# Kernel optimization log

Hardware: AMD Instinct MI355X
Metric: run time of the kernel (lower is better)

The kernel has to match this reference:

```python
import jax, jax.numpy as jnp
import numpy as np

B, J, PD = 4, 6890, 3
D, L, H, DH = 256, 4, 8, 64
INNER = H * DH          # 512
N = 2048                # downsample_dim (token count)
FF = 1024
M = 13780               # num_joints * upsample
HEAD_OUT = [3, 1, 3, 4, 3]  # mean3D, opacity, shs, rotations, scales


def setup_inputs() -> dict:
    ks = jax.random.split(jax.random.key(0), 16)
    rn = lambda k, shape, s=0.05: jax.random.normal(k, shape, jnp.float32) * s
    z = lambda shape: jnp.zeros(shape, jnp.float32)
    o = lambda shape: jnp.ones(shape, jnp.float32)
    return {
        'x': rn(ks[0], (B, J, PD), 1.0),
        'pre_emb_w': rn(ks[1], (PD, D)), 'pre_emb_b': z((D,)),
        'pre_conv_w': rn(ks[2], (N, J)), 'pre_conv_b': z((N,)),
        'pos_emb': rn(ks[3], (N, D), 0.02),
        'pre_norm_g': o((D,)), 'pre_norm_b': z((D,)),
        'ln1_g': o((L, D)), 'ln1_b': z((L, D)),
        'qkv_w': rn(ks[4], (L, D, 3 * INNER)),
        'out_w': rn(ks[5], (L, INNER, D)), 'out_b': z((L, D)),
        'ln2_g': o((L, D)), 'ln2_b': z((L, D)),
        'ff_w1': rn(ks[6], (L, D, FF)), 'ff_b1': z((L, FF)),
        'ff_w2': rn(ks[7], (L, FF, D)), 'ff_b2': z((L, D)),
        'up_w': rn(ks[8], (M, N)), 'up_b': z((M,)),
        'heads_w1': rn(ks[9], (5, D, D)), 'heads_b1': z((5, D)),
        'heads_w2': rn(ks[10], (5, D, 4)), 'heads_b2': z((5, 4)),
    }


def _ln(x, g, b, eps=1e-5):
    mu = jnp.mean(x, -1, keepdims=True)
    var = jnp.mean(jnp.square(x - mu), -1, keepdims=True)
    return (x - mu) * jax.lax.rsqrt(var + eps) * g + b


def _gelu(x):
    return jax.nn.gelu(x, approximate=False)  # torch nn.GELU default (erf)


def reference(x, pre_emb_w, pre_emb_b, pre_conv_w, pre_conv_b, pos_emb,
              pre_norm_g, pre_norm_b, ln1_g, ln1_b, qkv_w, out_w, out_b,
              ln2_g, ln2_b, ff_w1, ff_b1, ff_w2, ff_b2, up_w, up_b,
              heads_w1, heads_b1, heads_w2, heads_b2):
    scale = DH ** -0.5
    # token embedding: Linear(pose_dim->hidden) then Conv1d(num_joints->downsample_dim, k=1)
    h = x @ pre_emb_w + pre_emb_b                               # [B,J,D]
    h = jnp.einsum('bjd,nj->bnd', h, pre_conv_w) + pre_conv_b[None, :, None]  # [B,N,D]
    h = h + pos_emb[None]                                       # positional embedding
    h = _ln(h, pre_norm_g, pre_norm_b)
    # transformer encoder (pre-norm self-attn + FFN, residual)
    for i in range(L):
        y = _ln(h, ln1_g[i], ln1_b[i])
        qkv = y @ qkv_w[i]                                      # [B,N,3*INNER]
        q, k, v = jnp.split(qkv, 3, axis=-1)
        q = q.reshape(B, N, H, DH).transpose(0, 2, 1, 3)        # [B,H,N,DH]
        k = k.reshape(B, N, H, DH).transpose(0, 2, 1, 3)
        v = v.reshape(B, N, H, DH).transpose(0, 2, 1, 3)
        dots = jnp.einsum('bhnd,bhmd->bhnm', q, k) * scale      # [B,H,N,N]
        attn = jax.nn.softmax(dots, axis=-1)
        o = jnp.einsum('bhnm,bhmd->bhnd', attn, v)
        o = o.transpose(0, 2, 1, 3).reshape(B, N, INNER)
        h = o @ out_w[i] + out_b[i] + h
        y = _ln(h, ln2_g[i], ln2_b[i])
        h = _gelu(y @ ff_w1[i] + ff_b1[i]) @ ff_w2[i] + ff_b2[i] + h
    # upsample conv: Conv1d(downsample_dim -> num_joints*upsample, k=1)
    u = jnp.einsum('bnd,mn->bmd', h, up_w) + up_b[None, :, None]  # [B,M,D]
    # 5 gaussian-attribute heads (stacked; out dims padded to 4 and sliced)
    hid = _gelu(jnp.einsum('bmd,kde->kbme', u, heads_w1) + heads_b1[:, None, None, :])
    op = jnp.einsum('kbme,keo->kbmo', hid, heads_w2) + heads_b2[:, None, None, :]
    outs = [op[i, ..., :HEAD_OUT[i]] for i in range(5)]
    return jnp.concatenate(outs, axis=-1)                       # [B,M,14]
```

## Files before the change

kernel.cpp:

```cpp
#include <hip/hip_runtime.h>
#include <math.h>

#define B_ 4
#define J_ 6890
#define D_ 256
#define L_ 4
#define H_ 8
#define DH_ 64
#define INNER_ 512
#define N_ 2048
#define FF_ 1024
#define M_ 13780
#define MP_ 13824

typedef float4 f4;
typedef __attribute__((ext_vector_type(8))) short s16x8;
typedef __attribute__((ext_vector_type(4))) float fx4;

__device__ __forceinline__ float b2f(short s) {
    return __uint_as_float(((unsigned int)(unsigned short)s) << 16);
}
__device__ __forceinline__ short f2bf(float f) {
    unsigned int u = __float_as_uint(f);
    unsigned int r = (u + 0x7FFFu + ((u >> 16) & 1u)) >> 16;
    return (short)r;
}
__device__ __forceinline__ float gelu_f(float v) {
    return 0.5f * v * (1.0f + erff(v * 0.70710678118654752440f));
}

__device__ __forceinline__ void gld16(void* lds, const void* g) {
    __builtin_amdgcn_global_load_lds(
        (const __attribute__((address_space(1))) void*)g,
        (__attribute__((address_space(3))) void*)lds, 16, 0, 0);
}

__global__ __launch_bounds__(256) void embed_ln_kernel(
    const float* __restrict__ x, const float* __restrict__ emb_w,
    const float* __restrict__ emb_b, const float* __restrict__ conv_w,
    const float* __restrict__ conv_b, const float* __restrict__ pos_emb,
    const float* __restrict__ g, const float* __restrict__ beta,
    float* __restrict__ hout)
{
    const int n = blockIdx.x, b = blockIdx.y, t = threadIdx.x;
    const float* wrow = conv_w + (size_t)n * J_;
    const float* xb = x + (size_t)b * J_ * 3;
    float t0 = 0.f, t1 = 0.f, t2 = 0.f, s = 0.f;
    for (int j = t; j < J_; j += 256) {
        float w = wrow[j];
        s  += w;
        t0 += w * xb[3*j+0];
        t1 += w * xb[3*j+1];
        t2 += w * xb[3*j+2];
    }
    __shared__ float red[16];
    #pragma unroll
    for (int off = 32; off > 0; off >>= 1) {
        t0 += __shfl_down(t0, off, 64);
        t1 += __shfl_down(t1, off, 64);
        t2 += __shfl_down(t2, off, 64);
        s  += __shfl_down(s,  off, 64);
    }
    const int lane = t & 63, wid = t >> 6;
    if (lane == 0) { red[wid*4+0]=t0; red[wid*4+1]=t1; red[wid*4+2]=t2; red[wid*4+3]=s; }
    __syncthreads();
    t0 = red[0]+red[4]+red[8]+red[12];
    t1 = red[1]+red[5]+red[9]+red[13];
    t2 = red[2]+red[6]+red[10]+red[14];
    s  = red[3]+red[7]+red[11]+red[15];
    __syncthreads();

    float val = t0*emb_w[t] + t1*emb_w[D_+t] + t2*emb_w[2*D_+t]
              + s*emb_b[t] + conv_b[n] + pos_emb[(size_t)n*D_ + t];

    float sv = val, sq = val*val;
    #pragma unroll
    for (int off = 32; off > 0; off >>= 1) {
        sv += __shfl_down(sv, off, 64);
        sq += __shfl_down(sq, off, 64);
    }
    if (lane == 0) { red[wid*2]=sv; red[wid*2+1]=sq; }
    __syncthreads();
    sv = red[0]+red[2]+red[4]+red[6];
    sq = red[1]+red[3]+red[5]+red[7];
    float mu   = sv * (1.f/D_);
    float var  = sq * (1.f/D_) - mu*mu;
    float rstd = rsqrtf(fmaxf(var, 0.f) + 1e-5f);
    hout[((size_t)(b*N_ + n))*D_ + t] = (val - mu)*rstd*g[t] + beta[t];
}

__global__ __launch_bounds__(256) void ln_bf_kernel(
    const float* __restrict__ in, short* __restrict__ outp,
    const float* __restrict__ g, const float* __restrict__ beta)
{
    const int row = blockIdx.x, t = threadIdx.x;
    float v = in[(size_t)row*D_ + t];
    float sv = v, sq = v*v;
    #pragma unroll
    for (int off = 32; off > 0; off >>= 1) {
        sv += __shfl_down(sv, off, 64);
        sq += __shfl_down(sq, off, 64);
    }
    __shared__ float red[8];
    const int lane = t & 63, wid = t >> 6;
    if (lane == 0) { red[wid*2]=sv; red[wid*2+1]=sq; }
    __syncthreads();
    sv = red[0]+red[2]+red[4]+red[6];
    sq = red[1]+red[3]+red[5]+red[7];
    float mu   = sv * (1.f/D_);
    float var  = sq * (1.f/D_) - mu*mu;
    float rstd = rsqrtf(fmaxf(var, 0.f) + 1e-5f);
    outp[(size_t)row*D_ + t] = f2bf((v - mu)*rstd*g[t] + beta[t]);
}

__global__ __launch_bounds__(256) void tcvt_kernel(
    const float* __restrict__ in, short* __restrict__ outp,
    int R, int C, long inZ, long outZ)
{
    in   += (size_t)blockIdx.z * inZ;
    outp += (size_t)blockIdx.z * outZ;
    __shared__ float tile[32][33];
    const int c0 = blockIdx.x * 32, r0 = blockIdx.y * 32;
    const int t = threadIdx.x;
    const int row = t >> 3, c4 = (t & 7) * 4;
    f4 v = *(const f4*)&in[(size_t)(r0 + row)*C + c0 + c4];
    tile[row][c4+0] = v.x; tile[row][c4+1] = v.y;
    tile[row][c4+2] = v.z; tile[row][c4+3] = v.w;
    __syncthreads();
    const int oc = t >> 3, r4 = (t & 7) * 4;
    short* dst = &outp[(size_t)(c0 + oc)*R + r0 + r4];
    #pragma unroll
    for (int j = 0; j < 4; j++) dst[j] = f2bf(tile[r4 + j][oc]);
}

__global__ __launch_bounds__(256) void cvt_kernel(
    const float* __restrict__ in, short* __restrict__ outp)
{
    const size_t i = ((size_t)blockIdx.x * 256 + threadIdx.x) * 8;
    f4 a = *(const f4*)&in[i];
    f4 b = *(const f4*)&in[i + 4];
    s16x8 s;
    s[0]=f2bf(a.x); s[1]=f2bf(a.y); s[2]=f2bf(a.z); s[3]=f2bf(a.w);
    s[4]=f2bf(b.x); s[5]=f2bf(b.y); s[6]=f2bf(b.z); s[7]=f2bf(b.w);
    *(s16x8*)&outp[i] = s;
}

template<int BIAS_COL, int BIAS_ROW, int GELU, int RESID, int OUT_BF16>
__global__ __launch_bounds__(256) void gemm_bf16_kernel(
    const short* __restrict__ A, int lda, long sA,
    const short* __restrict__ Bt, int ldb, long sB,
    void* __restrict__ Cv, int ldc, long sC,
    const float* __restrict__ bias, long sBias,
    int M, int K)
{
    const int z = blockIdx.z;
    A  += (size_t)z * sA;
    Bt += (size_t)z * sB;
    const int m0 = blockIdx.y * 128, n0 = blockIdx.x * 128;
    const int t = threadIdx.x;
    const int lane = t & 63, w = t >> 6;
    const int wm = w >> 1, wn = w & 1;

    __shared__ short As[128*32];
    __shared__ short Bs[128*32];

    fx4 acc[4][4];
    #pragma unroll
    for (int i = 0; i < 4; i++)
        #pragma unroll
        for (int j = 0; j < 4; j++)
            acc[i][j] = (fx4){0.f, 0.f, 0.f, 0.f};

    const int srow = lane >> 2, scol = (lane & 3) * 8;
    const int fr = lane & 15, fg = (lane >> 4) * 8;

    for (int k0 = 0; k0 < K; k0 += 32) {
        __syncthreads();
        #pragma unroll
        for (int c = 0; c < 2; c++) {
            const int r = w*16 + c*64;
            gld16(&As[r*32], &A [(size_t)(m0 + r + srow)*lda + k0 + scol]);
            gld16(&Bs[r*32], &Bt[(size_t)(n0 + r + srow)*ldb + k0 + scol]);
        }
        __syncthreads();

        s16x8 af[4], bfr[4];
        #pragma unroll
        for (int i = 0; i < 4; i++) {
            af[i]  = *(const s16x8*)&As[(wm*64 + i*16 + fr)*32 + fg];
            bfr[i] = *(const s16x8*)&Bs[(wn*64 + i*16 + fr)*32 + fg];
        }
        #pragma unroll
        for (int i = 0; i < 4; i++)
            #pragma unroll
            for (int j = 0; j < 4; j++)
                acc[i][j] = __builtin_amdgcn_mfma_f32_16x16x32_bf16(
                                af[i], bfr[j], acc[i][j], 0, 0, 0);
    }

    const int cr = (lane >> 4) * 4, cc = lane & 15;
    #pragma unroll
    for (int i = 0; i < 4; i++) {
        #pragma unroll
        for (int j = 0; j < 4; j++) {
            const int gcol = n0 + wn*64 + j*16 + cc;
            #pragma unroll
            for (int r = 0; r < 4; r++) {
                const int grow = m0 + wm*64 + i*16 + cr + r;
                if (grow >= M) continue;
                float v = acc[i][j][r];
                if (BIAS_COL) v += bias[(size_t)z*sBias + gcol];
                if (BIAS_ROW) v += bias[(size_t)z*sBias + grow];
                if (GELU)     v = gelu_f(v);
                if (OUT_BF16) {
                    short* C = (short*)Cv + (size_t)z*sC;
                    C[(size_t)grow*ldc + gcol] = f2bf(v);
                } else {
                    float* C = (float*)Cv + (size_t)z*sC;
                    float* cp = &C[(size_t)grow*ldc + gcol];
                    float o = v;
                    if (RESID) o += *cp;
                    *cp = o;
                }
            }
        }
    }
}

__global__ __launch_bounds__(256) void attn_mfma_kernel(
    const short* __restrict__ qkv,
    short* __restrict__ o)
{
    const int q0 = blockIdx.x * 128;
    const int head = blockIdx.y;
    const int b = blockIdx.z;
    const int t = threadIdx.x;
    const int lane = t & 63, wq = t >> 6;
    const int g = lane >> 4, i16 = lane & 15;

    __shared__ short Kl[64*64];
    __shared__ short Vtl[64*64];
    __shared__ short Pl[128*64];
    char* const Kb = (char*)Kl;
    char* const Vb = (char*)Vtl;
    char* const Pb = (char*)Pl;

    s16x8 qreg[2][2];
    #pragma unroll
    for (int qf = 0; qf < 2; qf++) {
        const int qg = q0 + wq*32 + i16 + 16*qf;
        const short* qp = qkv + (size_t)(b*N_ + qg)*1536 + head*DH_;
        #pragma unroll
        for (int ks = 0; ks < 2; ks++)
            qreg[qf][ks] = *(const s16x8*)&qp[8*g + 32*ks];
    }

    fx4 oacc[4][2];
    #pragma unroll
    for (int df = 0; df < 4; df++)
        #pragma unroll
        for (int qf = 0; qf < 2; qf++)
            oacc[df][qf] = (fx4){0.f, 0.f, 0.f, 0.f};
    float mst[2] = {-INFINITY, -INFINITY};
    float lst[2] = {0.f, 0.f};

    const int sr = t >> 2, scol = (t & 3) * 16;
    const int swr = (sr & 7) << 4;
    const int qrow0 = wq*32 + i16, qrow1 = qrow0 + 16;
    const int swq0 = (qrow0 & 7) << 4, swq1 = (qrow1 & 7) << 4;

    for (int kt = 0; kt < N_/64; ++kt) {
        const short* kp = qkv + (size_t)(b*N_ + kt*64 + sr)*1536 + INNER_ + head*DH_ + scol;
        s16x8 k0 = *(const s16x8*)kp;
        s16x8 k1 = *(const s16x8*)(kp + 8);
        s16x8 v0 = *(const s16x8*)(kp + INNER_);
        s16x8 v1 = *(const s16x8*)(kp + INNER_ + 8);
        __syncthreads();
        *(s16x8*)(Kb + sr*128 + ((2*scol)      ^ swr)) = k0;
        *(s16x8*)(Kb + sr*128 + ((2*scol + 16) ^ swr)) = k1;
        #pragma unroll
        for (int j = 0; j < 8; j++) {
            *(short*)(Vb + (scol+j)*128   + ((2*sr) ^ (j<<4))) = v0[j];
            *(short*)(Vb + (scol+8+j)*128 + ((2*sr) ^ (j<<4))) = v1[j];
        }
        __syncthreads();

        fx4 sacc[4][2];
        #pragma unroll
        for (int kvf = 0; kvf < 4; kvf++)
            #pragma unroll
            for (int qf = 0; qf < 2; qf++)
                sacc[kvf][qf] = (fx4){0.f, 0.f, 0.f, 0.f};
        #pragma unroll
        for (int ks = 0; ks < 2; ks++) {
            #pragma unroll
            for (int kvf = 0; kvf < 4; kvf++) {
                const int kv = i16 + 16*kvf;
                s16x8 ka = *(const s16x8*)(Kb + kv*128 + ((16*g + 64*ks) ^ ((kv&7)<<4)));
                #pragma unroll
                for (int qf = 0; qf < 2; qf++)
                    sacc[kvf][qf] = __builtin_amdgcn_mfma_f32_16x16x32_bf16(
                                        ka, qreg[qf][ks], sacc[kvf][qf], 0, 0, 0);
            }
        }

        #pragma unroll
        for (int qf = 0; qf < 2; qf++) {
            float sv[16];
            #pragma unroll
            for (int kvf = 0; kvf < 4; kvf++)
                #pragma unroll
                for (int r = 0; r < 4; r++)
                    sv[kvf*4+r] = sacc[kvf][qf][r] * 0.125f;
            float tm = sv[0];
            #pragma unroll
            for (int k = 1; k < 16; k++) tm = fmaxf(tm, sv[k]);
            tm = fmaxf(tm, __shfl_xor(tm, 16, 64));
            tm = fmaxf(tm, __shfl_xor(tm, 32, 64));
            const float mn  = fmaxf(qf ? mst[1] : mst[0], tm);
            const float scl = __expf((qf ? mst[1] : mst[0]) - mn);
            float rs = 0.f;
            float p[16];
            #pragma unroll
            for (int k = 0; k < 16; k++) { p[k] = __expf(sv[k] - mn); rs += p[k]; }
            rs += __shfl_xor(rs, 16, 64);
            rs += __shfl_xor(rs, 32, 64);
            if (qf) { lst[1] = lst[1]*scl + rs; mst[1] = mn; }
            else    { lst[0] = lst[0]*scl + rs; mst[0] = mn; }
            #pragma unroll
            for (int df = 0; df < 4; df++) {
                oacc[df][qf][0] *= scl; oacc[df][qf][1] *= scl;
                oacc[df][qf][2] *= scl; oacc[df][qf][3] *= scl;
            }
            const int qr = qf ? qrow1 : qrow0;
            const int sq = qf ? swq1 : swq0;
            #pragma unroll
            for (int kvf = 0; kvf < 4; kvf++) {
                uint2 wv;
                wv.x = (unsigned int)(unsigned short)f2bf(p[4*kvf+0]) |
                       ((unsigned int)(unsigned short)f2bf(p[4*kvf+1]) << 16);
                wv.y = (unsigned int)(unsigned short)f2bf(p[4*kvf+2]) |
                       ((unsigned int)(unsigned short)f2bf(p[4*kvf+3]) << 16);
                *(uint2*)(Pb + qr*128 + ((8*g + 32*kvf) ^ sq)) = wv;
            }
        }

        asm volatile("s_waitcnt lgkmcnt(0)" ::: "memory");
        __builtin_amdgcn_sched_barrier(0);

        #pragma unroll
        for (int ks = 0; ks < 2; ks++) {
            s16x8 pf0 = *(const s16x8*)(Pb + qrow0*128 + ((16*g + 64*ks) ^ swq0));
            s16x8 pf1 = *(const s16x8*)(Pb + qrow1*128 + ((16*g + 64*ks) ^ swq1));
            #pragma unroll
            for (int df = 0; df < 4; df++) {
                const int dh = i16 + 16*df;
                s16x8 va = *(const s16x8*)(Vb + dh*128 + ((16*g + 64*ks) ^ ((dh&7)<<4)));
                oacc[df][0] = __builtin_amdgcn_mfma_f32_16x16x32_bf16(va, pf0, oacc[df][0], 0, 0, 0);
                oacc[df][1] = __builtin_amdgcn_mfma_f32_16x16x32_bf16(va, pf1, oacc[df][1], 0, 0, 0);
            }
        }
    }

    const float inv0 = 1.f / lst[0], inv1 = 1.f / lst[1];
    #pragma unroll
    for (int df = 0; df < 4; df++)
        #pragma unroll
        for (int r = 0; r < 4; r++) {
            const int dh = 4*g + r + 16*df;
            *(short*)(Pb + qrow0*128 + ((2*dh) ^ swq0)) = f2bf(oacc[df][0][r]*inv0);
            *(short*)(Pb + qrow1*128 + ((2*dh) ^ swq1)) = f2bf(oacc[df][1][r]*inv1);
        }
    __syncthreads();
    {
        const int qr = t >> 1, h2 = t & 1;
        const int sq = (qr & 7) << 4;
        short* op = o + (size_t)(b*N_ + q0 + qr)*INNER_ + head*DH_ + 32*h2;
        #pragma unroll
        for (int e = 0; e < 4; e++) {
            s16x8 vv = *(const s16x8*)(Pb + qr*128 + ((64*h2 + 16*e) ^ sq));
            *(s16x8*)&op[8*e] = vv;
        }
    }
}

__global__ __launch_bounds__(512) void heads_fused_kernel(
    const short* __restrict__ u,
    const short* __restrict__ w1T,
    const float* __restrict__ b1,
    const float* __restrict__ w2,
    const float* __restrict__ b2,
    float* __restrict__ outp)
{
    const int m0 = blockIdx.x * 128;
    const int b  = blockIdx.y;
    const int k  = blockIdx.z;
    const int t  = threadIdx.x;
    const int lane = t & 63, w = t >> 6;
    const int wm = w >> 2, wn = w & 3;

    __shared__ short As[128*32];
    __shared__ short Bs[256*32];
    __shared__ float w2s[1024];
    __shared__ float b1s[256];
    __shared__ float red4[4][128][4];

    if (t < 256) b1s[t] = b1[k*256 + t];
    w2s[t]       = w2[k*1024 + t];
    w2s[t + 512] = w2[k*1024 + t + 512];

    fx4 acc[4][4];
    #pragma unroll
    for (int i = 0; i < 4; i++)
        #pragma unroll
        for (int j = 0; j < 4; j++)
            acc[i][j] = (fx4){0.f, 0.f, 0.f, 0.f};

    const short* Ab = u + (size_t)b * 256;
    const short* Bb = w1T + (size_t)k * 65536;
    const int srow = lane >> 2, scol = (lane & 3) * 8;
    const int fr = lane & 15, fg = (lane >> 4) * 8;

    for (int k0 = 0; k0 < 256; k0 += 32) {
        __syncthreads();
        {
            const int r = w*16;
            gld16(&As[r*32], &Ab[(size_t)(m0 + r + srow)*1024 + k0 + scol]);
            gld16(&Bs[r*32],         &Bb[(size_t)(r + srow)*256 + k0 + scol]);
            gld16(&Bs[(128+r)*32],   &Bb[(size_t)(128 + r + srow)*256 + k0 + scol]);
        }
        __syncthreads();

        s16x8 af[4], bfr[4];
        #pragma unroll
        for (int i = 0; i < 4; i++) {
            af[i]  = *(const s16x8*)&As[(wm*64 + i*16 + fr)*32 + fg];
            bfr[i] = *(const s16x8*)&Bs[(wn*64 + i*16 + fr)*32 + fg];
        }
        #pragma unroll
        for (int i = 0; i < 4; i++)
            #pragma unroll
            for (int j = 0; j < 4; j++)
                acc[i][j] = __builtin_amdgcn_mfma_f32_16x16x32_bf16(
                                af[i], bfr[j], acc[i][j], 0, 0, 0);
    }

    const int cr = (lane >> 4) * 4, cc = lane & 15;
    float p[4][4][4];
    #pragma unroll
    for (int i = 0; i < 4; i++)
        #pragma unroll
        for (int r = 0; r < 4; r++)
            #pragma unroll
            for (int o = 0; o < 4; o++) p[i][r][o] = 0.f;

    #pragma unroll
    for (int i = 0; i < 4; i++) {
        #pragma unroll
        for (int j = 0; j < 4; j++) {
            const int col = wn*64 + j*16 + cc;
            const float bb = b1s[col];
            const float* wv = &w2s[col*4];
            #pragma unroll
            for (int r = 0; r < 4; r++) {
                const float hv = gelu_f(acc[i][j][r] + bb);
                #pragma unroll
                for (int o = 0; o < 4; o++) p[i][r][o] += hv * wv[o];
            }
        }
    }
    #pragma unroll
    for (int i = 0; i < 4; i++)
        #pragma unroll
        for (int r = 0; r < 4; r++)
            #pragma unroll
            for (int o = 0; o < 4; o++) {
                float v = p[i][r][o];
                v += __shfl_xor(v, 1, 64);
                v += __shfl_xor(v, 2, 64);
                v += __shfl_xor(v, 4, 64);
                v += __shfl_xor(v, 8, 64);
                p[i][r][o] = v;
            }
    if (cc == 0) {
        #pragma unroll
        for (int i = 0; i < 4; i++)
            #pragma unroll
            for (int r = 0; r < 4; r++)
                #pragma unroll
                for (int o = 0; o < 4; o++)
                    red4[wn][wm*64 + i*16 + cr + r][o] = p[i][r][o];
    }
    __syncthreads();

    const int koff = (k==0) ? 0 : (k==1) ? 3 : (k==2) ? 4 : (k==3) ? 7 : 11;
    const int kcnt = (k==1) ? 1 : (k==3) ? 4 : 3;
    {
        const int row = t >> 2, o = t & 3;
        const int m = m0 + row;
        if (o < kcnt && m < M_) {
            float v = red4[0][row][o] + red4[1][row][o]
                    + red4[2][row][o] + red4[3][row][o] + b2[k*4 + o];
            outp[((size_t)b*M_ + m)*14 + koff + o] = v;
        }
    }
}

extern "C" void kernel_launch(void* const* d_in, const int* in_sizes, int n_in,
                              void* d_out, int out_size, void* d_ws, size_t ws_size,
                              hipStream_t stream)
{
    const float* x          = (const float*)d_in[0];
    const float* pre_emb_w  = (const float*)d_in[1];
    const float* pre_emb_b  = (const float*)d_in[2];
    const float* pre_conv_w = (const float*)d_in[3];
    const float* pre_conv_b = (const float*)d_in[4];
    const float* pos_emb    = (const float*)d_in[5];
    const float* pre_norm_g = (const float*)d_in[6];
    const float* pre_norm_b = (const float*)d_in[7];
    const float* ln1_g      = (const float*)d_in[8];
    const float* ln1_b      = (const float*)d_in[9];
    const float* qkv_w      = (const float*)d_in[10];
    const float* out_w      = (const float*)d_in[11];
    const float* out_b      = (const float*)d_in[12];
    const float* ln2_g      = (const float*)d_in[13];
    const float* ln2_b      = (const float*)d_in[14];
    const float* ff_w1      = (const float*)d_in[15];
    const float* ff_b1      = (const float*)d_in[16];
    const float* ff_w2      = (const float*)d_in[17];
    const float* ff_b2      = (const float*)d_in[18];
    const float* up_w       = (const float*)d_in[19];
    const float* up_b       = (const float*)d_in[20];
    const float* heads_w1   = (const float*)d_in[21];
    const float* heads_b1   = (const float*)d_in[22];
    const float* heads_w2   = (const float*)d_in[23];
    const float* heads_b2   = (const float*)d_in[24];
    float* out = (float*)d_out;

    char* ws = (char*)d_ws;
    float* h      = (float*)(ws);
    char*  R2     = ws + 8388608;
    short* y_bf   = (short*)(R2);
    short* qkv_bf = (short*)(R2 + 4194304);
    short* ffmid  = qkv_bf;
    short* obuf   = (short*)(R2 + 29360128);
    short* qkvT   = (short*)(R2 + 37748736);
    short* outT   = (short*)(R2 + 40894464);
    short* ff1T   = (short*)(R2 + 41943040);
    short* ff2T   = (short*)(R2 + 44040192);
    short* upw_bf = (short*)(R2);
    short* hT     = (short*)(ws + 65011712);
    short* u_bf   = (short*)(ws + 69206016);
    short* w1T    = (short*)(ws + 97517568);

    tcvt_kernel<<<dim3(1536/32,  256/32, 4), 256, 0, stream>>>(qkv_w,    qkvT, 256, 1536, 256L*1536, 1536L*256);
    tcvt_kernel<<<dim3( 256/32,  512/32, 4), 256, 0, stream>>>(out_w,    outT, 512,  256, 512L*256,  256L*512);
    tcvt_kernel<<<dim3(1024/32,  256/32, 4), 256, 0, stream>>>(ff_w1,    ff1T, 256, 1024, 256L*1024, 1024L*256);
    tcvt_kernel<<<dim3( 256/32, 1024/32, 4), 256, 0, stream>>>(ff_w2,    ff2T, 1024, 256, 1024L*256, 256L*1024);
    tcvt_kernel<<<dim3( 256/32,  256/32, 5), 256, 0, stream>>>(heads_w1, w1T,  256,  256, 256L*256,  256L*256);

    embed_ln_kernel<<<dim3(N_, B_), 256, 0, stream>>>(
        x, pre_emb_w, pre_emb_b, pre_conv_w, pre_conv_b, pos_emb,
        pre_norm_g, pre_norm_b, h);

    const int rows = B_ * N_;
    for (int i = 0; i < L_; i++) {
        ln_bf_kernel<<<rows, 256, 0, stream>>>(h, y_bf, ln1_g + i*D_, ln1_b + i*D_);
        gemm_bf16_kernel<0,0,0,0,1><<<dim3(12, rows/128, 1), 256, 0, stream>>>(
            y_bf, 256, 0, qkvT + (size_t)i*1536*256, 256, 0,
            qkv_bf, 1536, 0, nullptr, 0, rows, 256);
        attn_mfma_kernel<<<dim3(N_/128, H_, B_), 256, 0, stream>>>(qkv_bf, obuf);
        gemm_bf16_kernel<1,0,0,1,0><<<dim3(2, rows/128, 1), 256, 0, stream>>>(
            obuf, 512, 0, outT + (size_t)i*256*512, 512, 0,
            h, 256, 0, out_b + i*D_, 0, rows, 512);
        ln_bf_kernel<<<rows, 256, 0, stream>>>(h, y_bf, ln2_g + i*D_, ln2_b + i*D_);
        gemm_bf16_kernel<1,0,1,0,1><<<dim3(8, rows/128, 1), 256, 0, stream>>>(
            y_bf, 256, 0, ff1T + (size_t)i*1024*256, 256, 0,
            ffmid, 1024, 0, ff_b1 + i*FF_, 0, rows, 256);
        gemm_bf16_kernel<1,0,0,1,0><<<dim3(2, rows/128, 1), 256, 0, stream>>>(
            ffmid, 1024, 0, ff2T + (size_t)i*256*1024, 1024, 0,
            h, 256, 0, ff_b2 + i*D_, 0, rows, 1024);
    }

    cvt_kernel<<<13780, 256, 0, stream>>>(up_w, upw_bf);
    tcvt_kernel<<<dim3(256/32, 2048/32, 4), 256, 0, stream>>>(h, hT, 2048, 256, 2048L*256, 256L*2048);
    gemm_bf16_kernel<0,1,0,0,1><<<dim3(8, MP_/128, 1), 256, 0, stream>>>(
        upw_bf, 2048, 0, hT, 2048, 0,
        u_bf, 1024, 0, up_b, 0, M_, 2048);

    heads_fused_kernel<<<dim3(MP_/128, B_, 5), 512, 0, stream>>>(
        u_bf, w1T, heads_b1, heads_w2, heads_b2, out);
}
```

Measured before the change: 1.605 ms.

## Use BK=64 swizzled LDS tiles in GEMMs and LDS-staged head reduction

Both the generic bf16 GEMM and the fused heads kernel now stage K-tiles of 64 instead of 32, with an XOR swizzle on the LDS column to avoid bank conflicts, halving the number of barrier pairs per K loop. The heads kernel also replaces the per-lane second-layer dot product and shuffle reduction with writing GELU hidden values as bf16 into a padded shared buffer that aliases the tile storage, then each thread reduces one row/output from LDS. This raises LDS usage per block (about 66KB in heads), which may lower occupancy, and rounds hidden activations to bf16 before the second layer.

```diff
diff --git a/kernel.cpp b/kernel.cpp
--- a/kernel.cpp
+++ b/kernel.cpp
@@ -161,8 +161,8 @@
     const int lane = t & 63, w = t >> 6;
     const int wm = w >> 1, wn = w & 1;
 
-    __shared__ short As[128*32];
-    __shared__ short Bs[128*32];
+    __shared__ short As[128*64];
+    __shared__ short Bs[128*64];
 
     fx4 acc[4][4];
     #pragma unroll
@@ -171,31 +171,37 @@
         for (int j = 0; j < 4; j++)
             acc[i][j] = (fx4){0.f, 0.f, 0.f, 0.f};
 
-    const int srow = lane >> 2, scol = (lane & 3) * 8;
-    const int fr = lane & 15, fg = (lane >> 4) * 8;
-
-    for (int k0 = 0; k0 < K; k0 += 32) {
+    const int srow = lane >> 3;
+    const int scol = ((lane & 7) ^ (lane >> 3)) * 8;
+    const int fr = lane & 15, g = lane >> 4;
+    const int fswz = (fr & 7) << 3;
+
+    for (int k0 = 0; k0 < K; k0 += 64) {
         __syncthreads();
         #pragma unroll
-        for (int c = 0; c < 2; c++) {
-            const int r = w*16 + c*64;
-            gld16(&As[r*32], &A [(size_t)(m0 + r + srow)*lda + k0 + scol]);
-            gld16(&Bs[r*32], &Bt[(size_t)(n0 + r + srow)*ldb + k0 + scol]);
+        for (int c = 0; c < 4; c++) {
+            const int r = w*32 + c*8;
+            gld16(&As[r*64], &A [(size_t)(m0 + r + srow)*lda + k0 + scol]);
+            gld16(&Bs[r*64], &Bt[(size_t)(n0 + r + srow)*ldb + k0 + scol]);
         }
         __syncthreads();
 
-        s16x8 af[4], bfr[4];
-        #pragma unroll
-        for (int i = 0; i < 4; i++) {
-            af[i]  = *(const s16x8*)&As[(wm*64 + i*16 + fr)*32 + fg];
-            bfr[i] = *(const s16x8*)&Bs[(wn*64 + i*16 + fr)*32 + fg];
-        }
-        #pragma unroll
-        for (int i = 0; i < 4; i++)
-            #pragma unroll
-            for (int j = 0; j < 4; j++)
-                acc[i][j] = __builtin_amdgcn_mfma_f32_16x16x32_bf16(
-                                af[i], bfr[j], acc[i][j], 0, 0, 0);
+        #pragma unroll
+        for (int ks = 0; ks < 2; ks++) {
+            const int co = (ks*32 + g*8) ^ fswz;
+            s16x8 af[4], bfr[4];
+            #pragma unroll
+            for (int i = 0; i < 4; i++) {
+                af[i]  = *(const s16x8*)&As[(wm*64 + i*16 + fr)*64 + co];
+                bfr[i] = *(const s16x8*)&Bs[(wn*64 + i*16 + fr)*64 + co];
+            }
+            #pragma unroll
+            for (int i = 0; i < 4; i++)
+                #pragma unroll
+                for (int j = 0; j < 4; j++)
+                    acc[i][j] = __builtin_amdgcn_mfma_f32_16x16x32_bf16(
+                                    af[i], bfr[j], acc[i][j], 0, 0, 0);
+        }
     }
 
     const int cr = (lane >> 4) * 4, cc = lane & 15;
@@ -399,11 +405,12 @@
     const int lane = t & 63, w = t >> 6;
     const int wm = w >> 2, wn = w & 3;
 
-    __shared__ short As[128*32];
-    __shared__ short Bs[256*32];
+    __shared__ char hbuf[67584];
+    short* const As  = (short*)hbuf;
+    short* const Bs  = (short*)(hbuf + 16384);
+    short* const hid = (short*)hbuf;
     __shared__ float w2s[1024];
     __shared__ float b1s[256];
-    __shared__ float red4[4][128][4];
 
     if (t < 256) b1s[t] = b1[k*256 + t];
     w2s[t]       = w2[k*1024 + t];
@@ -418,78 +425,57 @@
 
     const short* Ab = u + (size_t)b * 256;
     const short* Bb = w1T + (size_t)k * 65536;
-    const int srow = lane >> 2, scol = (lane & 3) * 8;
-    const int fr = lane & 15, fg = (lane >> 4) * 8;
-
-    for (int k0 = 0; k0 < 256; k0 += 32) {
+    const int srow = lane >> 3;
+    const int scol = ((lane & 7) ^ (lane >> 3)) * 8;
+    const int fr = lane & 15, g = lane >> 4;
+    const int fswz = (fr & 7) << 3;
+
+    for (int k0 = 0; k0 < 256; k0 += 64) {
         __syncthreads();
         {
-            const int r = w*16;
-            gld16(&As[r*32], &Ab[(size_t)(m0 + r + srow)*1024 + k0 + scol]);
-            gld16(&Bs[r*32],         &Bb[(size_t)(r + srow)*256 + k0 + scol]);
-            gld16(&Bs[(128+r)*32],   &Bb[(size_t)(128 + r + srow)*256 + k0 + scol]);
+            const int ra0 = w*16;
+            gld16(&As[ra0*64],      &Ab[(size_t)(m0 + ra0 + srow)*1024 + k0 + scol]);
+            gld16(&As[(ra0+8)*64],  &Ab[(size_t)(m0 + ra0 + 8 + srow)*1024 + k0 + scol]);
+            #pragma unroll
+            for (int c = 0; c < 4; c++) {
+                const int rb = w*32 + c*8;
+                gld16(&Bs[rb*64], &Bb[(size_t)(rb + srow)*256 + k0 + scol]);
+            }
         }
         __syncthreads();
 
-        s16x8 af[4], bfr[4];
-        #pragma unroll
-        for (int i = 0; i < 4; i++) {
-            af[i]  = *(const s16x8*)&As[(wm*64 + i*16 + fr)*32 + fg];
-            bfr[i] = *(const s16x8*)&Bs[(wn*64 + i*16 + fr)*32 + fg];
-        }
-        #pragma unroll
-        for (int i = 0; i < 4; i++)
-            #pragma unroll
-            for (int j = 0; j < 4; j++)
-                acc[i][j] = __builtin_amdgcn_mfma_f32_16x16x32_bf16(
-                                af[i], bfr[j], acc[i][j], 0, 0, 0);
-    }
+        #pragma unroll
+        for (int ks = 0; ks < 2; ks++) {
+            const int co = (ks*32 + g*8) ^ fswz;
+            s16x8 af[4], bfr[4];
+            #pragma unroll
+            for (int i = 0; i < 4; i++) {
+                af[i]  = *(const s16x8*)&As[(wm*64 + i*16 + fr)*64 + co];
+                bfr[i] = *(const s16x8*)&Bs[(wn*64 + i*16 + fr)*64 + co];
+            }
+            #pragma unroll
+            for (int i = 0; i < 4; i++)
+                #pragma unroll
+                for (int j = 0; j < 4; j++)
+                    acc[i][j] = __builtin_amdgcn_mfma_f32_16x16x32_bf16(
+                                    af[i], bfr[j], acc[i][j], 0, 0, 0);
+        }
+    }
+    __syncthreads();
 
     const int cr = (lane >> 4) * 4, cc = lane & 15;
-    float p[4][4][4];
-    #pragma unroll
-    for (int i = 0; i < 4; i++)
-        #pragma unroll
-        for (int r = 0; r < 4; r++)
-            #pragma unroll
-            for (int o = 0; o < 4; o++) p[i][r][o] = 0.f;
-
     #pragma unroll
     for (int i = 0; i < 4; i++) {
         #pragma unroll
         for (int j = 0; j < 4; j++) {
             const int col = wn*64 + j*16 + cc;
             const float bb = b1s[col];
-            const float* wv = &w2s[col*4];
             #pragma unroll
             for (int r = 0; r < 4; r++) {
-                const float hv = gelu_f(acc[i][j][r] + bb);
-                #pragma unroll
-                for (int o = 0; o < 4; o++) p[i][r][o] += hv * wv[o];
-            }
-        }
-    }
-    #pragma unroll
-    for (int i = 0; i < 4; i++)
-        #pragma unroll
-        for (int r = 0; r < 4; r++)
-            #pragma unroll
-            for (int o = 0; o < 4; o++) {
-                float v = p[i][r][o];
-                v += __shfl_xor(v, 1, 64);
-                v += __shfl_xor(v, 2, 64);
-                v += __shfl_xor(v, 4, 64);
-                v += __shfl_xor(v, 8, 64);
-                p[i][r][o] = v;
-            }
-    if (cc == 0) {
-        #pragma unroll
-        for (int i = 0; i < 4; i++)
-            #pragma unroll
-            for (int r = 0; r < 4; r++)
-                #pragma unroll
-                for (int o = 0; o < 4; o++)
-                    red4[wn][wm*64 + i*16 + cr + r][o] = p[i][r][o];
+                const int row = wm*64 + i*16 + cr + r;
+                hid[row*260 + col] = f2bf(gelu_f(acc[i][j][r] + bb));
+            }
+        }
     }
     __syncthreads();
 
@@ -497,12 +483,19 @@
     const int kcnt = (k==1) ? 1 : (k==3) ? 4 : 3;
     {
         const int row = t >> 2, o = t & 3;
+        float a = 0.f;
+        const short* hrow = &hid[row*260];
+        #pragma unroll 8
+        for (int c4 = 0; c4 < 64; c4++) {
+            uint2 hv = *(const uint2*)&hrow[c4*4];
+            a += b2f((short)(hv.x & 0xFFFF))       * w2s[(c4*4+0)*4 + o];
+            a += b2f((short)(hv.x >> 16))          * w2s[(c4*4+1)*4 + o];
+            a += b2f((short)(hv.y & 0xFFFF))       * w2s[(c4*4+2)*4 + o];
+            a += b2f((short)(hv.y >> 16))          * w2s[(c4*4+3)*4 + o];
+        }
         const int m = m0 + row;
-        if (o < kcnt && m < M_) {
-            float v = red4[0][row][o] + red4[1][row][o]
-                    + red4[2][row][o] + red4[3][row][o] + b2[k*4 + o];
-            outp[((size_t)b*M_ + m)*14 + koff + o] = v;
-        }
+        if (o < kcnt && m < M_)
+            outp[((size_t)b*M_ + m)*14 + koff + o] = a + b2[k*4 + o];
     }
 }
 
```

Result: faster. 1.350 ms (-15.9%).
